# Kernel optimization log

Measured on AMD Instinct MI355X. Metric: run time of the kernel, lower is better.

Reference implementation:

```python
import jax, jax.numpy as jnp
import numpy as np

HIDDEN = 512

def setup_inputs() -> dict:
    key = jax.random.key(0)
    kx, kq, kk, kv = jax.random.split(key, 4)
    B, S, H = 4, 4096, HIDDEN
    scale = 1.0 / np.sqrt(H)
    x = jax.random.normal(kx, (B, S, H), dtype=jnp.float32)
    # nn.Linear weights are [out, in]; y = x @ W.T
    Wq = jax.random.normal(kq, (H, H), dtype=jnp.float32) * scale
    Wk = jax.random.normal(kk, (H, H), dtype=jnp.float32) * scale
    Wv = jax.random.normal(kv, (H, H), dtype=jnp.float32) * scale
    return {"x": x, "Wq": Wq, "Wk": Wk, "Wv": Wv}

def reference(x, Wq, Wk, Wv):
    H = x.shape[-1]
    q = jnp.einsum('bsh,oh->bso', x, Wq)
    k = jnp.einsum('bsh,oh->bso', x, Wk)
    v = jnp.einsum('bsh,oh->bso', x, Wv)
    scores = jnp.einsum('bqh,bkh->bqk', q, k) / jnp.sqrt(jnp.asarray(H, x.dtype))
    att = jax.nn.softmax(scores, axis=-1)  # max-subtracted softmax, same math as manual version
    return jnp.einsum('bqk,bkh->bqh', att, v)
```

## Files before the change

kernel.cpp:

```cpp
#include <hip/hip_runtime.h>
#include <stdint.h>

typedef unsigned short u16;
typedef __bf16  bf16x8   __attribute__((ext_vector_type(8)));
typedef float   floatx4  __attribute__((ext_vector_type(4)));
typedef unsigned short ushortx4 __attribute__((ext_vector_type(4)));

__device__ __forceinline__ u16 f2bf(float f) {
  unsigned u = __builtin_bit_cast(unsigned, f);
  u += 0x7FFFu + ((u >> 16) & 1u);
  return (u16)(u >> 16);
}

#define GLD_LDS16(g, l)                                                        \
  __builtin_amdgcn_global_load_lds(                                            \
      (const __attribute__((address_space(1))) void*)(g),                      \
      (__attribute__((address_space(3))) void*)(l), 16, 0, 0)

#define VMW(N) asm volatile("s_waitcnt vmcnt(" #N ")" ::: "memory")

__global__ __launch_bounds__(256) void cvt_w(
    const float* __restrict__ Wq, const float* __restrict__ Wk,
    const float* __restrict__ Wv, u16* __restrict__ dst)
{
  const int z = blockIdx.y;
  const float* src = (z == 0) ? Wq : (z == 1) ? Wk : Wv;
  u16* d = dst + (size_t)z * 262144;
  const int idx = (blockIdx.x * 256 + threadIdx.x) * 8;
  const float4 lo = *(const float4*)&src[idx];
  const float4 hi = *(const float4*)&src[idx + 4];
  union { u16 h[8]; uint4 v; } pk;
  pk.h[0] = f2bf(lo.x); pk.h[1] = f2bf(lo.y); pk.h[2] = f2bf(lo.z); pk.h[3] = f2bf(lo.w);
  pk.h[4] = f2bf(hi.x); pk.h[5] = f2bf(hi.y); pk.h[6] = f2bf(hi.z); pk.h[7] = f2bf(hi.w);
  *(uint4*)&d[idx] = pk.v;
}

__global__ __launch_bounds__(256) void cvt_x(
    const float* __restrict__ X, u16* __restrict__ dst)
{
  const int idx = (blockIdx.x * 256 + threadIdx.x) * 8;
  const float4 lo = *(const float4*)&X[idx];
  const float4 hi = *(const float4*)&X[idx + 4];
  union { u16 h[8]; uint4 v; } pk;
  pk.h[0] = f2bf(lo.x); pk.h[1] = f2bf(lo.y); pk.h[2] = f2bf(lo.z); pk.h[3] = f2bf(lo.w);
  pk.h[4] = f2bf(hi.x); pk.h[5] = f2bf(hi.y); pk.h[6] = f2bf(hi.z); pk.h[7] = f2bf(hi.w);
  *(uint4*)&dst[idx] = pk.v;
}

__global__ __launch_bounds__(512, 2) void qkv8(
    const u16* __restrict__ X16, const u16* __restrict__ Wb,
    u16* __restrict__ qo, u16* __restrict__ ko, u16* __restrict__ vto)
{
  __shared__ u16 lds[65536];

  const int tid = threadIdx.x;
  const int w  = tid >> 6, l = tid & 63;
  const int lr = l & 15, lq = l >> 4;
  const int wA = (w & 1) * 16;
  const int wB = (w >> 1) * 16;

  const int bx = blockIdx.x;
  const int li = (bx & 7) * 48 + (bx >> 3);
  const int z  = li >> 7, u = li & 127;

  const u16* Ag; const u16* Bg; u16* dst; float sc; size_t ostr; int mb, nb;
  if (z < 2) {
    Ag = Wb + (size_t)z * 262144; Bg = X16;
    dst = z ? ko : qo; sc = z ? 1.0f : 0.06375871732f; ostr = 512;
    mb = (u & 1) * 256;  nb = (u >> 1) * 256;
  } else {
    Ag = X16; Bg = Wb + (size_t)2 * 262144;
    dst = vto; sc = 1.0f; ostr = 16384;
    mb = (u >> 1) * 256; nb = (u & 1) * 256;
  }

  floatx4 acc[8][4];
  const floatx4 fz = {0.f, 0.f, 0.f, 0.f};
#pragma unroll
  for (int i = 0; i < 8; ++i)
#pragma unroll
    for (int j = 0; j < 4; ++j) acc[i][j] = fz;

  auto stage = [&](int s) {
    const int ts = s >> 2, kind = s & 3;
    const int mat = kind & 1, h = kind >> 1;
    const u16* src = mat ? Bg : Ag;
    const int rbase = mat ? nb : mb;
    u16* dstl = &lds[(ts & 1) * 32768 + mat * 16384];
#pragma unroll
    for (int i = 0; i < 2; ++i) {
      const int c = i * 512 + tid;
      const int r = h * 128 + (c >> 3), k16 = c & 7;
      const int k16s = k16 ^ (r & 7);
      GLD_LDS16(src + (size_t)(rbase + r) * 512 + ts * 64 + k16s * 8,
                &dstl[r * 64 + k16 * 8]);
    }
  };

#pragma unroll
  for (int s = 0; s < 6; ++s) stage(s);
  VMW(4);
  __builtin_amdgcn_s_barrier();
  __builtin_amdgcn_sched_barrier(0);

  bf16x8 af[4][2];
  bf16x8 bf0[2][2], bf1[2][2];

#pragma unroll
  for (int t = 0; t < 8; ++t) {
#pragma unroll
    for (int qd = 0; qd < 4; ++qd) {
      const int fmh = qd >> 1;
      const int fnh = fmh ^ (qd & 1);
      const u16* AB = &lds[(t & 1) * 32768];
      const u16* BB = AB + 16384;

      if (qd == 0 || qd == 2) {
#pragma unroll
        for (int im = 0; im < 4; ++im) {
          const int rA = (fmh * 4 + im) * 32 + wA + lr;
#pragma unroll
          for (int ks = 0; ks < 2; ++ks) {
            const int k16p = (ks * 4 + lq) ^ (rA & 7);
            af[im][ks] = *(const bf16x8*)&AB[rA * 64 + k16p * 8];
          }
        }
      }
      if (qd == 0) {
#pragma unroll
        for (int jn = 0; jn < 2; ++jn) {
          const int rB = jn * 64 + wB + lr;
#pragma unroll
          for (int ks = 0; ks < 2; ++ks) {
            const int k16p = (ks * 4 + lq) ^ (rB & 7);
            bf0[jn][ks] = *(const bf16x8*)&BB[rB * 64 + k16p * 8];
          }
        }
      }
      if (qd == 1) {
#pragma unroll
        for (int jn = 0; jn < 2; ++jn) {
          const int rB = (2 + jn) * 64 + wB + lr;
#pragma unroll
          for (int ks = 0; ks < 2; ++ks) {
            const int k16p = (ks * 4 + lq) ^ (rB & 7);
            bf1[jn][ks] = *(const bf16x8*)&BB[rB * 64 + k16p * 8];
          }
        }
      }

      const int s = t * 4 + qd + 6;
      if (s < 32) stage(s);

      __builtin_amdgcn_sched_barrier(0);
      __builtin_amdgcn_s_barrier();
      asm volatile("s_waitcnt lgkmcnt(0)" ::: "memory");
      __builtin_amdgcn_sched_barrier(0);

      __builtin_amdgcn_s_setprio(1);
      if (fnh) {
#pragma unroll
        for (int im = 0; im < 4; ++im)
#pragma unroll
          for (int jn = 0; jn < 2; ++jn)
#pragma unroll
            for (int ks = 0; ks < 2; ++ks)
              acc[fmh * 4 + im][2 + jn] =
                  __builtin_amdgcn_mfma_f32_16x16x32_bf16(
                      af[im][ks], bf1[jn][ks], acc[fmh * 4 + im][2 + jn], 0, 0, 0);
      } else {
#pragma unroll
        for (int im = 0; im < 4; ++im)
#pragma unroll
          for (int jn = 0; jn < 2; ++jn)
#pragma unroll
            for (int ks = 0; ks < 2; ++ks)
              acc[fmh * 4 + im][jn] =
                  __builtin_amdgcn_mfma_f32_16x16x32_bf16(
                      af[im][ks], bf0[jn][ks], acc[fmh * 4 + im][jn], 0, 0, 0);
      }
      __builtin_amdgcn_s_setprio(0);

      if (qd == 3) {
        if (t < 6)        VMW(4);
        else if (t == 6)  VMW(0);
      }
      __builtin_amdgcn_s_barrier();
      __builtin_amdgcn_sched_barrier(0);
    }
  }

  const int cr = lq * 4;
#pragma unroll
  for (int fm = 0; fm < 8; ++fm)
#pragma unroll
    for (int fn = 0; fn < 4; ++fn) {
      const int mv = mb + fm * 32 + wA + cr;
      const int nv = nb + fn * 64 + wB + lr;
      ushortx4 pk;
#pragma unroll
      for (int r = 0; r < 4; ++r) pk[r] = f2bf(acc[fm][fn][r] * sc);
      *(ushortx4*)&dst[(size_t)nv * ostr + mv] = pk;
    }
}

#define QK_READ_A(BUFP, HALF)                                                  \
  do {                                                                         \
    const u16* AB_ = &lds[(BUFP) * 32768];                                     \
    _Pragma("unroll")                                                          \
    for (int im_ = 0; im_ < 4; ++im_) {                                        \
      const int rA_ = ((HALF) * 4 + im_) * 32 + wA + lr;                       \
      _Pragma("unroll")                                                        \
      for (int ks_ = 0; ks_ < 2; ++ks_) {                                      \
        const int kp_ = (ks_ * 4 + lq) ^ (rA_ & 7);                            \
        af[im_][ks_] = *(const bf16x8*)&AB_[rA_ * 64 + kp_ * 8];               \
      }                                                                        \
    }                                                                          \
  } while (0)

#define QK_READ_B(BUFP, HALF, DST)                                             \
  do {                                                                         \
    const u16* BB_ = &lds[(BUFP) * 32768 + 16384];                             \
    _Pragma("unroll")                                                          \
    for (int jn_ = 0; jn_ < 2; ++jn_) {                                        \
      const int rB_ = ((HALF) * 2 + jn_) * 64 + wB + lr;                       \
      _Pragma("unroll")                                                        \
      for (int ks_ = 0; ks_ < 2; ++ks_) {                                      \
        const int kp_ = (ks_ * 4 + lq) ^ (rB_ & 7);                            \
        DST[jn_][ks_] = *(const bf16x8*)&BB_[rB_ * 64 + kp_ * 8];              \
      }                                                                        \
    }                                                                          \
  } while (0)

__global__ __launch_bounds__(512, 2) void qk_exp8(
    const u16* __restrict__ q, const u16* __restrict__ k,
    u16* __restrict__ S, float* __restrict__ lsum)
{
  __shared__ u16 lds[65536];

  const int tid = threadIdx.x;
  const int w  = tid >> 6, l = tid & 63;
  const int lr = l & 15, lq = l >> 4;
  const int wA = (w & 1) * 16;
  const int wB = (w >> 1) * 16;
  const int kb0 = blockIdx.x * 256;
  const int qb0 = blockIdx.y * 256;
  const int b   = blockIdx.z;
  const size_t rb = (size_t)b * 4096;
  const u16* kg = k + rb * 512;
  const u16* qg = q + rb * 512;

  floatx4 acc[8][4];
  const floatx4 fz = {0.f, 0.f, 0.f, 0.f};
#pragma unroll
  for (int i = 0; i < 8; ++i)
#pragma unroll
    for (int j = 0; j < 4; ++j) acc[i][j] = fz;

  auto stage = [&](int s) {
    const int ts = s >> 2, kind = s & 3;
    const int mat = kind & 1, h = kind >> 1;
    const u16* src = mat ? qg : kg;
    const int rbase = mat ? qb0 : kb0;
    u16* dst = &lds[(ts & 1) * 32768 + mat * 16384];
#pragma unroll
    for (int i = 0; i < 2; ++i) {
      const int c = i * 512 + tid;
      const int r = h * 128 + (c >> 3), k16 = c & 7;
      const int k16s = k16 ^ (r & 7);
      GLD_LDS16(src + (size_t)(rbase + r) * 512 + ts * 64 + k16s * 8,
                &dst[r * 64 + k16 * 8]);
    }
  };

  bf16x8 af[4][2];
  bf16x8 bf0[2][2], bf1[2][2];

#pragma unroll
  for (int s = 0; s < 6; ++s) stage(s);
  VMW(4);
  __builtin_amdgcn_s_barrier();
  __builtin_amdgcn_sched_barrier(0);
  QK_READ_A(0, 0);
  QK_READ_B(0, 0, bf0);

#pragma unroll
  for (int t = 0; t < 8; ++t) {
#pragma unroll
    for (int qd = 0; qd < 4; ++qd) {
      const int fmh = qd >> 1;
      const int fnh = fmh ^ (qd & 1);

      __builtin_amdgcn_s_setprio(1);
      if (fnh) {
#pragma unroll
        for (int im = 0; im < 4; ++im)
#pragma unroll
          for (int jn = 0; jn < 2; ++jn)
#pragma unroll
            for (int ks = 0; ks < 2; ++ks)
              acc[fmh * 4 + im][2 + jn] =
                  __builtin_amdgcn_mfma_f32_16x16x32_bf16(
                      af[im][ks], bf1[jn][ks], acc[fmh * 4 + im][2 + jn], 0, 0, 0);
      } else {
#pragma unroll
        for (int im = 0; im < 4; ++im)
#pragma unroll
          for (int jn = 0; jn < 2; ++jn)
#pragma unroll
            for (int ks = 0; ks < 2; ++ks)
              acc[fmh * 4 + im][jn] =
                  __builtin_amdgcn_mfma_f32_16x16x32_bf16(
                      af[im][ks], bf0[jn][ks], acc[fmh * 4 + im][jn], 0, 0, 0);
      }
      __builtin_amdgcn_s_setprio(0);
      __builtin_amdgcn_sched_barrier(0);

      if (qd == 0) QK_READ_B(t & 1, 1, bf1);
      if (qd == 1) QK_READ_A(t & 1, 1);
      if (qd == 3 && t < 7) {
        QK_READ_A((t + 1) & 1, 0);
        QK_READ_B((t + 1) & 1, 0, bf0);
      }

      const int s = t * 4 + qd + 6;
      if (s < 32) stage(s);

      if (qd == 2) { if (t < 6) VMW(6); else if (t == 6) VMW(4); }
      if (qd == 3) { if (t < 6) VMW(4); else if (t == 6) VMW(0); }

      __builtin_amdgcn_sched_barrier(0);
      if (t < 7 || qd < 3) __builtin_amdgcn_s_barrier();
      __builtin_amdgcn_sched_barrier(0);
    }
  }

  const int cr = lq * 4;
  u16* Sb = S + ((size_t)b << 24);
  float js[4] = {0.f, 0.f, 0.f, 0.f};
#pragma unroll
  for (int fm = 0; fm < 8; ++fm)
#pragma unroll
    for (int fn = 0; fn < 4; ++fn) {
      const int key = kb0 + fm * 32 + wA + cr;
      const int qr  = qb0 + fn * 64 + wB + lr;
      ushortx4 pk;
      float s4 = 0.f;
#pragma unroll
      for (int r = 0; r < 4; ++r) {
        const float p = __builtin_amdgcn_exp2f(acc[fm][fn][r] - 17.31234049f);
        s4 += p;
        pk[r] = f2bf(p);
      }
      js[fn] += s4;
      *(ushortx4*)&Sb[(size_t)qr * 4096 + key] = pk;
    }
#pragma unroll
  for (int fn = 0; fn < 4; ++fn) {
    float s = js[fn];
    s += __shfl_xor(s, 16);
    s += __shfl_xor(s, 32);
    if (lq == 0)
      atomicAdd(&lsum[rb + qb0 + fn * 64 + wB + lr], s);
  }
}

#define PV_STG_A(TT, CK) do {                                                  \
    u16* dA_ = &lds[((TT) & 1) * 24576];                                       \
    _Pragma("unroll")                                                          \
    for (int i_ = 0; i_ < 2; ++i_) {                                           \
      const int c_ = i_ * 512 + tid, r_ = c_ >> 3, k_ = c_ & 7;                \
      GLD_LDS16(Sb + (size_t)(lm0 + (CK) * 128 + r_) * 4096 + (TT) * 64 +      \
                    (k_ ^ (r_ & 7)) * 8,                                       \
                &dA_[((CK) * 128 + r_) * 64 + k_ * 8]);                        \
    }                                                                          \
  } while (0)

#define PV_STG_B(TT) do {                                                      \
    u16* dB_ = &lds[((TT) & 1) * 24576 + 16384];                               \
    _Pragma("unroll")                                                          \
    for (int i_ = 0; i_ < 2; ++i_) {                                           \
      const int c_ = i_ * 512 + tid, r_ = c_ >> 3, k_ = c_ & 7;                \
      GLD_LDS16(vt + (size_t)(n0 + r_) * 16384 + bofs + (TT) * 64 +            \
                    (k_ ^ (r_ & 7)) * 8,                                       \
                &dB_[r_ * 64 + k_ * 8]);                                       \
    }                                                                          \
  } while (0)

#define PV_PH(T, PH, STAGE_CODE, TAIL_CODE) do {                               \
    const u16* AB_ = &lds[((T) & 1) * 24576];                                  \
    const u16* BB_ = AB_ + 16384;                                              \
    _Pragma("unroll")                                                          \
    for (int im_ = 0; im_ < 4; ++im_) {                                        \
      const int rA_ = ((PH) * 4 + im_) * 32 + wm16 + lr;                       \
      _Pragma("unroll")                                                        \
      for (int ks_ = 0; ks_ < 2; ++ks_) {                                      \
        const int kp_ = (ks_ * 4 + lq) ^ (rA_ & 7);                            \
        af[im_][ks_] = *(const bf16x8*)&AB_[rA_ * 64 + kp_ * 8];               \
      }                                                                        \
    }                                                                          \
    if ((PH) == 0) {                                                           \
      _Pragma("unroll")                                                        \
      for (int jn_ = 0; jn_ < 2; ++jn_) {                                      \
        const int rB_ = wn32 + jn_ * 16 + lr;                                  \
        _Pragma("unroll")                                                      \
        for (int ks_ = 0; ks_ < 2; ++ks_) {                                    \
          const int kp_ = (ks_ * 4 + lq) ^ (rB_ & 7);                          \
          bfv[jn_][ks_] = *(const bf16x8*)&BB_[rB_ * 64 + kp_ * 8];            \
        }                                                                      \
      }                                                                        \
    }                                                                          \
    STAGE_CODE;                                                                \
    __builtin_amdgcn_sched_barrier(0);                                         \
    __builtin_amdgcn_s_barrier();                                              \
    asm volatile("s_waitcnt lgkmcnt(0)" ::: "memory");                         \
    __builtin_amdgcn_sched_barrier(0);                                         \
    __builtin_amdgcn_s_setprio(1);                                             \
    _Pragma("unroll")                                                          \
    for (int im_ = 0; im_ < 4; ++im_)                                          \
      _Pragma("unroll")                                                        \
      for (int jn_ = 0; jn_ < 2; ++jn_)                                        \
        _Pragma("unroll")                                                      \
        for (int ks_ = 0; ks_ < 2; ++ks_)                                      \
          acc[(PH) * 4 + im_][jn_] = __builtin_amdgcn_mfma_f32_16x16x32_bf16(  \
              af[im_][ks_], bfv[jn_][ks_], acc[(PH) * 4 + im_][jn_], 0, 0, 0); \
    __builtin_amdgcn_s_setprio(0);                                             \
    TAIL_CODE;                                                                 \
    __builtin_amdgcn_s_barrier();                                              \
    __builtin_amdgcn_sched_barrier(0);                                         \
  } while (0)

#define PV_TILE(T, G_A1, G_A0B, VMCODE) do {                                   \
    PV_PH(T, 0, { if (G_A1) PV_STG_A((T) + 1, 1); }, (void)0);                 \
    PV_PH(T, 1, { if (G_A0B) { PV_STG_A((T) + 2, 0); PV_STG_B((T) + 2); } },   \
          VMCODE);                                                             \
  } while (0)

__global__ __launch_bounds__(512, 2) void pv8(
    const u16* __restrict__ S, const u16* __restrict__ vt,
    const float* __restrict__ lsum, float* __restrict__ out)
{
  __shared__ u16 lds[49152];

  const int tid = threadIdx.x;
  const int w  = tid >> 6, l = tid & 63;
  const int lr = l & 15, lq = l >> 4;
  const int wm16 = (w & 1) * 16;
  const int wn32 = (w >> 1) * 32;

  const int wg = blockIdx.x;
  const int li = (wg & 7) * 32 + (wg >> 3);
  const int n0 = (li & 3) * 128;
  const int m0 = (li >> 2) * 256;
  const int b  = m0 >> 12;
  const int lm0 = m0 & 4095;
  const u16* Sb = S + ((size_t)b << 24);
  const size_t bofs = (size_t)b * 4096;

  floatx4 acc[8][2];
  const floatx4 fz = {0.f, 0.f, 0.f, 0.f};
#pragma unroll
  for (int i = 0; i < 8; ++i) { acc[i][0] = fz; acc[i][1] = fz; }

  bf16x8 af[4][2], bfv[2][2];

  PV_STG_A(0, 0); PV_STG_B(0); PV_STG_A(0, 1); PV_STG_A(1, 0); PV_STG_B(1);
  VMW(4);
  __builtin_amdgcn_s_barrier();
  __builtin_amdgcn_sched_barrier(0);

  for (int t = 0; t < 62; t += 2) {
    PV_TILE(t,     1, 1, VMW(4));
    PV_TILE(t + 1, 1, 1, VMW(4));
  }
  PV_TILE(62, 1, 0, VMW(0));
  PV_TILE(63, 0, 0, (void)0);

  const int cr = lq * 4;
#pragma unroll
  for (int fm = 0; fm < 8; ++fm) {
    const int m = m0 + fm * 32 + wm16 + cr;
    float inv[4];
#pragma unroll
    for (int r = 0; r < 4; ++r) inv[r] = 1.0f / lsum[m + r];
#pragma unroll
    for (int jn = 0; jn < 2; ++jn) {
      const int n = n0 + wn32 + jn * 16 + lr;
#pragma unroll
      for (int r = 0; r < 4; ++r)
        out[(size_t)(m + r) * 512 + n] = acc[fm][jn][r] * inv[r];
    }
  }
}

extern "C" void kernel_launch(void* const* d_in, const int* in_sizes, int n_in,
                              void* d_out, int out_size, void* d_ws, size_t ws_size,
                              hipStream_t stream) {
  (void)in_sizes; (void)n_in; (void)out_size; (void)ws_size;
  const float* x  = (const float*)d_in[0];
  const float* Wq = (const float*)d_in[1];
  const float* Wk = (const float*)d_in[2];
  const float* Wv = (const float*)d_in[3];
  float* out = (float*)d_out;
  u16* ws  = (u16*)d_ws;
  u16* qw  = ws;
  u16* kw  = qw + (size_t)16384 * 512;
  u16* vw  = kw + (size_t)16384 * 512;
  u16* x16 = vw + (size_t)16384 * 512;
  u16* wb  = x16 + (size_t)16384 * 512;
  u16* Sp  = wb + (size_t)3 * 262144;
  float* lsum = (float*)(Sp + ((size_t)4 << 24));

  hipMemsetAsync(lsum, 0, 16384 * sizeof(float), stream);
  cvt_w<<<dim3(128, 3), dim3(256), 0, stream>>>(Wq, Wk, Wv, wb);
  cvt_x<<<dim3(4096), dim3(256), 0, stream>>>(x, x16);
  qkv8<<<dim3(384), dim3(512), 0, stream>>>(x16, wb, qw, kw, vw);
  qk_exp8<<<dim3(16, 16, 4), dim3(512), 0, stream>>>(qw, kw, Sp, lsum);
  pv8<<<dim3(256), dim3(512), 0, stream>>>(Sp, vw, lsum, out);
}
```

Measured before the change: 300.0 us.

## Shrink QK tile to 256x128 with 32-wide K steps for higher occupancy

Restructures the QK^T+exp kernel so each block covers 256 keys by 128 queries instead of 256x256. The K step narrows from 64 to 32, LDS falls from 128KB to 48KB, and the grid doubles. Launch bounds rise to 4 blocks per CU and the swizzle and staging schedule are rewritten to match. The goal is more resident waves to hide latency and fewer registers per thread, at the cost of less reuse of each K tile and more barriers per unit of work.

```diff
diff --git a/kernel.cpp b/kernel.cpp
--- a/kernel.cpp
+++ b/kernel.cpp
@@ -204,39 +204,43 @@
     }
 }
 
+#define QK_MFMA(FMH)                                                           \
+  do {                                                                         \
+    _Pragma("unroll")                                                          \
+    for (int im_ = 0; im_ < 4; ++im_)                                          \
+      _Pragma("unroll")                                                        \
+      for (int fn_ = 0; fn_ < 2; ++fn_)                                        \
+        acc[(FMH) * 4 + im_][fn_] = __builtin_amdgcn_mfma_f32_16x16x32_bf16(   \
+            af[im_], bfv[fn_], acc[(FMH) * 4 + im_][fn_], 0, 0, 0);            \
+  } while (0)
+
 #define QK_READ_A(BUFP, HALF)                                                  \
   do {                                                                         \
-    const u16* AB_ = &lds[(BUFP) * 32768];                                     \
+    const u16* AB_ = &lds[(BUFP) * 12288];                                     \
     _Pragma("unroll")                                                          \
     for (int im_ = 0; im_ < 4; ++im_) {                                        \
       const int rA_ = ((HALF) * 4 + im_) * 32 + wA + lr;                       \
-      _Pragma("unroll")                                                        \
-      for (int ks_ = 0; ks_ < 2; ++ks_) {                                      \
-        const int kp_ = (ks_ * 4 + lq) ^ (rA_ & 7);                            \
-        af[im_][ks_] = *(const bf16x8*)&AB_[rA_ * 64 + kp_ * 8];               \
-      }                                                                        \
-    }                                                                          \
-  } while (0)
-
-#define QK_READ_B(BUFP, HALF, DST)                                             \
+      const int kp_ = lq ^ ((rA_ >> 1) & 3);                                   \
+      af[im_] = *(const bf16x8*)&AB_[rA_ * 32 + kp_ * 8];                      \
+    }                                                                          \
+  } while (0)
+
+#define QK_READ_B(BUFP)                                                        \
   do {                                                                         \
-    const u16* BB_ = &lds[(BUFP) * 32768 + 16384];                             \
-    _Pragma("unroll")                                                          \
-    for (int jn_ = 0; jn_ < 2; ++jn_) {                                        \
-      const int rB_ = ((HALF) * 2 + jn_) * 64 + wB + lr;                       \
-      _Pragma("unroll")                                                        \
-      for (int ks_ = 0; ks_ < 2; ++ks_) {                                      \
-        const int kp_ = (ks_ * 4 + lq) ^ (rB_ & 7);                            \
-        DST[jn_][ks_] = *(const bf16x8*)&BB_[rB_ * 64 + kp_ * 8];              \
-      }                                                                        \
-    }                                                                          \
-  } while (0)
-
-__global__ __launch_bounds__(512, 2) void qk_exp8(
+    const u16* BB_ = &lds[(BUFP) * 12288 + 8192];                              \
+    _Pragma("unroll")                                                          \
+    for (int fn_ = 0; fn_ < 2; ++fn_) {                                        \
+      const int rB_ = fn_ * 64 + wB + lr;                                      \
+      const int kp_ = lq ^ ((rB_ >> 1) & 3);                                   \
+      bfv[fn_] = *(const bf16x8*)&BB_[rB_ * 32 + kp_ * 8];                     \
+    }                                                                          \
+  } while (0)
+
+__global__ __launch_bounds__(512, 4) void qk_exp8(
     const u16* __restrict__ q, const u16* __restrict__ k,
     u16* __restrict__ S, float* __restrict__ lsum)
 {
-  __shared__ u16 lds[65536];
+  __shared__ u16 lds[24576];
 
   const int tid = threadIdx.x;
   const int w  = tid >> 6, l = tid & 63;
@@ -244,104 +248,78 @@
   const int wA = (w & 1) * 16;
   const int wB = (w >> 1) * 16;
   const int kb0 = blockIdx.x * 256;
-  const int qb0 = blockIdx.y * 256;
+  const int qb0 = blockIdx.y * 128;
   const int b   = blockIdx.z;
   const size_t rb = (size_t)b * 4096;
   const u16* kg = k + rb * 512;
   const u16* qg = q + rb * 512;
 
-  floatx4 acc[8][4];
+  floatx4 acc[8][2];
   const floatx4 fz = {0.f, 0.f, 0.f, 0.f};
 #pragma unroll
-  for (int i = 0; i < 8; ++i)
-#pragma unroll
-    for (int j = 0; j < 4; ++j) acc[i][j] = fz;
-
-  auto stage = [&](int s) {
-    const int ts = s >> 2, kind = s & 3;
-    const int mat = kind & 1, h = kind >> 1;
-    const u16* src = mat ? qg : kg;
-    const int rbase = mat ? qb0 : kb0;
-    u16* dst = &lds[(ts & 1) * 32768 + mat * 16384];
+  for (int i = 0; i < 8; ++i) { acc[i][0] = fz; acc[i][1] = fz; }
+
+  auto stageA = [&](int ts) {
+    u16* dst = &lds[(ts & 1) * 12288];
 #pragma unroll
     for (int i = 0; i < 2; ++i) {
       const int c = i * 512 + tid;
-      const int r = h * 128 + (c >> 3), k16 = c & 7;
-      const int k16s = k16 ^ (r & 7);
-      GLD_LDS16(src + (size_t)(rbase + r) * 512 + ts * 64 + k16s * 8,
-                &dst[r * 64 + k16 * 8]);
+      const int r = c >> 2, k16 = c & 3;
+      GLD_LDS16(kg + (size_t)(kb0 + r) * 512 + ts * 32 +
+                    (k16 ^ ((r >> 1) & 3)) * 8,
+                &dst[r * 32 + k16 * 8]);
     }
   };
-
-  bf16x8 af[4][2];
-  bf16x8 bf0[2][2], bf1[2][2];
-
-#pragma unroll
-  for (int s = 0; s < 6; ++s) stage(s);
-  VMW(4);
+  auto stageB = [&](int ts) {
+    u16* dst = &lds[(ts & 1) * 12288 + 8192];
+    const int r = tid >> 2, k16 = tid & 3;
+    GLD_LDS16(qg + (size_t)(qb0 + r) * 512 + ts * 32 +
+                  (k16 ^ ((r >> 1) & 3)) * 8,
+              &dst[r * 32 + k16 * 8]);
+  };
+
+  bf16x8 af[4], bfv[2];
+
+  stageA(0); stageB(0); stageB(1); stageA(1);
+  VMW(3);
   __builtin_amdgcn_s_barrier();
-  __builtin_amdgcn_sched_barrier(0);
   QK_READ_A(0, 0);
-  QK_READ_B(0, 0, bf0);
-
-#pragma unroll
-  for (int t = 0; t < 8; ++t) {
-#pragma unroll
-    for (int qd = 0; qd < 4; ++qd) {
-      const int fmh = qd >> 1;
-      const int fnh = fmh ^ (qd & 1);
-
-      __builtin_amdgcn_s_setprio(1);
-      if (fnh) {
-#pragma unroll
-        for (int im = 0; im < 4; ++im)
-#pragma unroll
-          for (int jn = 0; jn < 2; ++jn)
-#pragma unroll
-            for (int ks = 0; ks < 2; ++ks)
-              acc[fmh * 4 + im][2 + jn] =
-                  __builtin_amdgcn_mfma_f32_16x16x32_bf16(
-                      af[im][ks], bf1[jn][ks], acc[fmh * 4 + im][2 + jn], 0, 0, 0);
-      } else {
-#pragma unroll
-        for (int im = 0; im < 4; ++im)
-#pragma unroll
-          for (int jn = 0; jn < 2; ++jn)
-#pragma unroll
-            for (int ks = 0; ks < 2; ++ks)
-              acc[fmh * 4 + im][jn] =
-                  __builtin_amdgcn_mfma_f32_16x16x32_bf16(
-                      af[im][ks], bf0[jn][ks], acc[fmh * 4 + im][jn], 0, 0, 0);
-      }
-      __builtin_amdgcn_s_setprio(0);
+  QK_READ_B(0);
+
+#pragma unroll
+  for (int t = 0; t < 16; ++t) {
+    __builtin_amdgcn_s_setprio(1);
+    QK_MFMA(0);
+    __builtin_amdgcn_s_setprio(0);
+    __builtin_amdgcn_sched_barrier(0);
+    QK_READ_A(t & 1, 1);
+    if (t + 2 <= 15) stageB(t + 2);
+    if (t < 14) VMW(1);
+    else if (t == 14) VMW(0);
+    __builtin_amdgcn_sched_barrier(0);
+    __builtin_amdgcn_s_barrier();
+    __builtin_amdgcn_sched_barrier(0);
+
+    __builtin_amdgcn_s_setprio(1);
+    QK_MFMA(1);
+    __builtin_amdgcn_s_setprio(0);
+    __builtin_amdgcn_sched_barrier(0);
+    if (t < 15) { QK_READ_A((t + 1) & 1, 0); QK_READ_B((t + 1) & 1); }
+    if (t + 2 <= 15) stageA(t + 2);
+    if (t < 15) {
       __builtin_amdgcn_sched_barrier(0);
-
-      if (qd == 0) QK_READ_B(t & 1, 1, bf1);
-      if (qd == 1) QK_READ_A(t & 1, 1);
-      if (qd == 3 && t < 7) {
-        QK_READ_A((t + 1) & 1, 0);
-        QK_READ_B((t + 1) & 1, 0, bf0);
-      }
-
-      const int s = t * 4 + qd + 6;
-      if (s < 32) stage(s);
-
-      if (qd == 2) { if (t < 6) VMW(6); else if (t == 6) VMW(4); }
-      if (qd == 3) { if (t < 6) VMW(4); else if (t == 6) VMW(0); }
-
-      __builtin_amdgcn_sched_barrier(0);
-      if (t < 7 || qd < 3) __builtin_amdgcn_s_barrier();
+      __builtin_amdgcn_s_barrier();
       __builtin_amdgcn_sched_barrier(0);
     }
   }
 
   const int cr = lq * 4;
   u16* Sb = S + ((size_t)b << 24);
-  float js[4] = {0.f, 0.f, 0.f, 0.f};
+  float js[2] = {0.f, 0.f};
 #pragma unroll
   for (int fm = 0; fm < 8; ++fm)
 #pragma unroll
-    for (int fn = 0; fn < 4; ++fn) {
+    for (int fn = 0; fn < 2; ++fn) {
       const int key = kb0 + fm * 32 + wA + cr;
       const int qr  = qb0 + fn * 64 + wB + lr;
       ushortx4 pk;
@@ -356,7 +334,7 @@
       *(ushortx4*)&Sb[(size_t)qr * 4096 + key] = pk;
     }
 #pragma unroll
-  for (int fn = 0; fn < 4; ++fn) {
+  for (int fn = 0; fn < 2; ++fn) {
     float s = js[fn];
     s += __shfl_xor(s, 16);
     s += __shfl_xor(s, 32);
@@ -515,6 +493,6 @@
   cvt_w<<<dim3(128, 3), dim3(256), 0, stream>>>(Wq, Wk, Wv, wb);
   cvt_x<<<dim3(4096), dim3(256), 0, stream>>>(x, x16);
   qkv8<<<dim3(384), dim3(512), 0, stream>>>(x16, wb, qw, kw, vw);
-  qk_exp8<<<dim3(16, 16, 4), dim3(512), 0, stream>>>(qw, kw, Sp, lsum);
+  qk_exp8<<<dim3(16, 32, 4), dim3(512), 0, stream>>>(qw, kw, Sp, lsum);
   pv8<<<dim3(256), dim3(512), 0, stream>>>(Sp, vw, lsum, out);
 }
```

After: 307.5 us. +2.5%, slower.
